# Kernel optimization log

Hardware: AMD Instinct MI355X
Metric: run time of the kernel (lower is better)

The kernel has to match this reference:

```python
import jax, jax.numpy as jnp
import numpy as np


def setup_inputs() -> dict:
    key = jax.random.key(0)
    ks = jax.random.split(key, 6)
    B, C, H, W, Q = 16, 64, 64, 64, 8192
    HID = 256
    K = C * 9  # 576, unfolded channel count and srnet out_dim (co_mat=1)
    feat = jax.random.normal(ks[0], (B, C, H, W), jnp.float32)
    coord = jax.random.uniform(ks[1], (B, Q, 2), jnp.float32) * 2.0 - 1.0  # normalized [-1,1]
    cell = jnp.ones((B, Q, 2), jnp.float32) * (2.0 / 128.0)  # HR cell size for 128-px grid
    w1 = jax.random.normal(ks[2], (3, HID), jnp.float32) / np.sqrt(3.0)
    b1 = jnp.zeros((HID,), jnp.float32)
    w2 = jax.random.normal(ks[3], (HID, HID), jnp.float32) / np.sqrt(float(HID))
    b2 = jnp.zeros((HID,), jnp.float32)
    w3 = jax.random.normal(ks[4], (HID, K), jnp.float32) / np.sqrt(float(HID))
    b3 = jnp.zeros((K,), jnp.float32)
    return {"feat": feat, "coord": coord, "cell": cell,
            "w1": w1, "b1": b1, "w2": w2, "b2": b2, "w3": w3, "b3": b3}


def reference(feat, coord, cell, w1, b1, w2, b2, w3, b3):
    B, C, H, W = feat.shape
    Q = coord.shape[1]
    K = C * 9
    co_mat = 1
    # F.unfold(feat, 3, padding=1).view(B, C*9, H, W): channel-major, kernel pos minor
    padded = jnp.pad(feat, ((0, 0), (0, 0), (1, 1), (1, 1)))
    patches = jnp.stack([padded[:, :, i:i + H, j:j + W]
                         for i in range(3) for j in range(3)], axis=2)  # [B,C,9,H,W]
    featu = patches.reshape(B, K, H * W)
    # shift query coords by half a cell
    coord_ = coord - cell / 2.0
    coord_q = jnp.clip(coord_ + 1e-6, -1.0 + 1e-6, 1.0 - 1e-6)
    # nearest grid_sample, align_corners=False: idx = round(((c+1)*S - 1)/2)
    # coord[...,0] indexes H (grid y after flip), coord[...,1] indexes W (grid x)
    iy = jnp.clip(jnp.round(((coord_q[..., 0] + 1.0) * H - 1.0) / 2.0), 0, H - 1).astype(jnp.int32)
    ix = jnp.clip(jnp.round(((coord_q[..., 1] + 1.0) * W - 1.0) / 2.0), 0, W - 1).astype(jnp.int32)
    lin = iy * W + ix  # [B,Q]
    q_feat = jnp.take_along_axis(featu, lin[:, None, :], axis=2).transpose(0, 2, 1)  # [B,Q,K]
    # q_coord: make_coord value minus half-pixel shift at the nearest index = 2i/S - 1 (exact)
    qy = 2.0 * iy.astype(jnp.float32) / H - 1.0
    qx = 2.0 * ix.astype(jnp.float32) / W - 1.0
    rel_y = (coord_[..., 0] - qy) * (H / 2.0)
    rel_x = (coord_[..., 1] - qx) * (W / 2.0)
    r_rev = cell[..., 0] * (H / 2.0)
    inp = jnp.stack([rel_y, rel_x, r_rev], axis=-1)  # [B,Q,3]
    # srnet MLP: per-query filter of shape [K, co_mat]
    h = jax.nn.relu(inp @ w1 + b1)
    h = jax.nn.relu(h @ w2 + b2)
    wmat = (h @ w3 + b3).reshape(B, Q, K, co_mat)
    # bmm combine: [1,K] @ [K,co_mat] per query
    pred = jnp.einsum('bqk,bqkc->bqc', q_feat, wmat)  # [B,Q,1]
    return pred
```

## Files before the change

kernel.cpp:

```cpp
#include <hip/hip_runtime.h>
#include <hip/hip_bf16.h>

#define BB 16
#define CC 64
#define HH 64
#define WW 64
#define QQ 8192
#define HID 256
#define KK 576
#define HT 66
#define FROW 264

typedef short short8 __attribute__((ext_vector_type(8)));
typedef short sv4    __attribute__((ext_vector_type(4)));
typedef float f32x4  __attribute__((ext_vector_type(4)));

__device__ __forceinline__ short f2bf(float f) {
    union { float f; unsigned u; } v; v.f = f;
    unsigned r = v.u + 0x7fffu + ((v.u >> 16) & 1u);
    return (short)(r >> 16);
}
__device__ __forceinline__ float bf2f(short s) {
    union { unsigned u; float f; } v; v.u = ((unsigned)(unsigned short)s) << 16;
    return v.f;
}
__device__ __forceinline__ void barrier_lds() {
    asm volatile("s_waitcnt lgkmcnt(0)" ::: "memory");
    __builtin_amdgcn_s_barrier();
    asm volatile("" ::: "memory");
}
__device__ __forceinline__ void glld16(const short* g, short* l) {
    __builtin_amdgcn_global_load_lds(
        (const __attribute__((address_space(1))) void*)g,
        (__attribute__((address_space(3))) void*)l, 16, 0, 0);
}

__global__ __launch_bounds__(256) void prep_transpose_k(const float* __restrict__ feat,
                                                        const float* __restrict__ w2,
                                                        const float* __restrict__ w3,
                                                        const float* __restrict__ b3,
                                                        short* __restrict__ featT,
                                                        short* __restrict__ w3cB,
                                                        short* __restrict__ w2cB) {
    __shared__ float ftile[64][65];
    const int t = threadIdx.x;
    const int gidx = blockIdx.x * 256 + t;

    if (gidx < 156672) {
        int kchunk = gidx / 2176;
        int rem = gidx - kchunk * 2176;
        int n = rem >> 3, j = rem & 7;
        int kglob = kchunk * 8 + j;
        int pos = kglob >> 6, c = kglob & 63;
        float v = 0.f;
        if (n < 256)      v = w3[n * KK + c * 9 + pos];
        else if (n == 256) v = b3[c * 9 + pos];
        w3cB[gidx] = f2bf(v);
    }
    if (gidx < 65536) {
        int kchunk = gidx >> 11;
        int rem = gidx & 2047;
        int n = rem >> 3, j = rem & 7;
        int k = kchunk * 8 + j;
        w2cB[gidx] = f2bf(w2[k * 256 + n]);
    }

    const int x = blockIdx.x & 7;
    const int i = blockIdx.x >> 3;
    const int b  = (i < 66) ? (x + 8) : x;
    const int yy = (i < 66) ? i : (i - 66);
    short* out_row = featT + ((b * HT + yy) * HT) * 64;

    if (yy == 0 || yy == HT - 1) {
        for (int idx = t; idx < HT * 64; idx += 256) out_row[idx] = 0;
        return;
    }
    const int y = yy - 1;
    const float* src = feat + ((b * CC) * HH + y) * WW;
#pragma unroll
    for (int i2 = 0; i2 < 16; ++i2) {
        int idx = i2 * 256 + t;
        int c = idx >> 6, xx = idx & 63;
        ftile[c][xx] = src[c * (HH * WW) + xx];
    }
    if (t < 64) out_row[t] = 0;
    else if (t < 128) out_row[(HT - 1) * 64 + (t - 64)] = 0;
    __syncthreads();
#pragma unroll
    for (int i2 = 0; i2 < 16; ++i2) {
        int idx = i2 * 256 + t;
        int xx = idx >> 6, c = idx & 63;
        out_row[(xx + 1) * 64 + c] = f2bf(ftile[c][xx]);
    }
}

#define SSTR 72
__global__ __launch_bounds__(256, 2) void conv_k(const short* __restrict__ featT,
                                                 const short* __restrict__ w3cB,
                                                 short* __restrict__ F) {
    __shared__ short slab[3 * HT * SSTR];
    const int t = threadIdx.x;
    const int wave = t >> 6, lane = t & 63, quad = lane >> 4, ln16 = lane & 15;
    const int x = blockIdx.x & 7;
    const int i0 = blockIdx.x >> 3;
    const int b = (i0 < 64) ? (x + 8) : x;
    const int y = i0 & 63;

    f32x4 acc[4][5];
#pragma unroll
    for (int a = 0; a < 4; ++a)
#pragma unroll
        for (int i = 0; i < 5; ++i) acc[a][i] = (f32x4){0.f, 0.f, 0.f, 0.f};

    short8 bbuf[3][5];
    const short* bbase = w3cB + (quad * 272 + ln16) * 8;
    auto loadB = [&](int st, int slot) {
#pragma unroll
        for (int i = 0; i < 5; ++i) {
            int sub = (i < 4) ? (wave + 4 * i) : 16;
            bbuf[slot][i] = *(const short8*)(bbase + st * 8704 + sub * 128);
        }
    };

    loadB(0, 0);
    loadB(1, 1);

    const short* slabsrc = featT + b * (HT * HT * 64) + y * (HT * 64);
#pragma unroll
    for (int it = 0; it < 7; ++it) {
        int i = it * 256 + t;
        if (i < 1584) {
            short8 v = *(const short8*)(slabsrc + i * 8);
            int row = i >> 3, cs = (i & 7) * 8;
            *(short8*)(&slab[row * SSTR + cs]) = v;
        }
    }
    barrier_lds();

#pragma unroll
    for (int st = 0; st < 18; ++st) {
        if (st < 16) loadB(st + 2, (st + 2) % 3);
        const int pos = st >> 1, ks = st & 1;
        const int di = pos / 3, dj = pos - di * 3;
        short8 af[4];
#pragma unroll
        for (int ms = 0; ms < 4; ++ms)
            af[ms] = *(const short8*)(&slab[(di * HT + ms * 16 + ln16 + dj) * SSTR + ks * 32 + quad * 8]);
#pragma unroll
        for (int i = 0; i < 5; ++i)
#pragma unroll
            for (int ms = 0; ms < 4; ++ms)
                acc[ms][i] = __builtin_amdgcn_mfma_f32_16x16x32_bf16(af[ms], bbuf[st % 3][i], acc[ms][i], 0, 0, 0);
    }

#pragma unroll
    for (int h = 0; h < 2; ++h) {
        if (h) barrier_lds();
#pragma unroll
        for (int i = 0; i < 5; ++i) {
            int sub = (i < 4) ? (wave + 4 * i) : 16;
            int n = sub * 16 + ln16;
            bool store = (i < 4) || (wave == 0 && n < FROW);
            if (store) {
#pragma unroll
                for (int ms2 = 0; ms2 < 2; ++ms2) {
                    int ms = h * 2 + ms2;
#pragma unroll
                    for (int r = 0; r < 4; ++r) {
                        int xl = ms2 * 16 + quad * 4 + r;
                        slab[xl * FROW + n] = f2bf(acc[ms][i][r]);
                    }
                }
            }
        }
        barrier_lds();
        short8* dst = (short8*)(F + ((long)(b * 64 + y) * 64 + h * 32) * FROW);
        const short8* src8 = (const short8*)slab;
#pragma unroll
        for (int it = 0; it < 5; ++it) {
            int idx = it * 256 + t;
            if (idx < (32 * FROW) / 8) dst[idx] = src8[idx];
        }
    }
}

__global__ __launch_bounds__(256, 2) void mlp_k(const float* __restrict__ coord,
                                                const float* __restrict__ cell,
                                                const float* __restrict__ w1,
                                                const float* __restrict__ b1,
                                                const float* __restrict__ b2v,
                                                const short* __restrict__ w2cB,
                                                const short* __restrict__ F,
                                                float* __restrict__ out) {
    __shared__ short HhF[16384];
    __shared__ short FLds[16384];

    const int t = threadIdx.x;
    const int wave = t >> 6, lane = t & 63, quad = lane >> 4, ln16 = lane & 15;
    const int xcd = blockIdx.x & 7;
    const int i0 = blockIdx.x >> 3;
    const int b  = (i0 < 128) ? xcd : (xcd + 8);
    const int qi = i0 & 127;
    const int qbase = b * QQ + qi * 64;

    const int g = qbase + lane;
    const float2 cc = *(const float2*)(coord + g * 2);
    const float2 ce = *(const float2*)(cell + g * 2);

    short8 wbuf[8][4];
    const short* w2base = w2cB + (quad * 256 + wave * 64 + ln16) * 8;
#pragma unroll
    for (int s = 0; s < 8; ++s)
#pragma unroll
        for (int i = 0; i < 4; ++i)
            wbuf[s][i] = *(const short8*)(w2base + s * 8192 + i * 128);
    __builtin_amdgcn_sched_barrier(0);

    const float coy = cc.x - ce.x * 0.5f, cox = cc.y - ce.y * 0.5f;
    const float cqy = fminf(fmaxf(coy + 1e-6f, -0.999999f), 0.999999f);
    const float cqx = fminf(fmaxf(cox + 1e-6f, -0.999999f), 0.999999f);
    int iy = (int)rintf(((cqy + 1.0f) * 64.0f - 1.0f) * 0.5f); iy = min(max(iy, 0), 63);
    int ix = (int)rintf(((cqx + 1.0f) * 64.0f - 1.0f) * 0.5f); ix = min(max(ix, 0), 63);
    const int lin = iy * 64 + ix;
    const float in0 = (coy - ((float)iy * (1.0f / 32.0f) - 1.0f)) * 32.0f;
    const float in1 = (cox - ((float)ix * (1.0f / 32.0f) - 1.0f)) * 32.0f;
    const float in2 = ce.x * 32.0f;

    short8 hv[8];
    const int k0w = wave * 64;
#pragma unroll
    for (int c8 = 0; c8 < 8; ++c8) {
        const int k0 = k0w + c8 * 8;
        f32x4 wa0 = *(const f32x4*)(w1 + k0),       wa1 = *(const f32x4*)(w1 + k0 + 4);
        f32x4 wb0 = *(const f32x4*)(w1 + 256 + k0), wb1 = *(const f32x4*)(w1 + 256 + k0 + 4);
        f32x4 wc0 = *(const f32x4*)(w1 + 512 + k0), wc1 = *(const f32x4*)(w1 + 512 + k0 + 4);
        f32x4 bb0 = *(const f32x4*)(b1 + k0),       bb1 = *(const f32x4*)(b1 + k0 + 4);
#pragma unroll
        for (int jj = 0; jj < 4; ++jj) {
            float v0 = fmaf(in0, wa0[jj], fmaf(in1, wb0[jj], fmaf(in2, wc0[jj], bb0[jj])));
            float v1 = fmaf(in0, wa1[jj], fmaf(in1, wb1[jj], fmaf(in2, wc1[jj], bb1[jj])));
            hv[c8][jj]     = f2bf(fmaxf(v0, 0.f));
            hv[c8][jj + 4] = f2bf(fmaxf(v1, 0.f));
        }
    }
#pragma unroll
    for (int c8 = 0; c8 < 8; ++c8)
        *(short8*)(&HhF[((2 * wave + (c8 >> 2)) * 4 + (c8 & 3)) * 512 + lane * 8]) = hv[c8];
    __builtin_amdgcn_sched_barrier(0);

    const short* Fb = F + (long)b * 4096 * FROW;
    const short fbs = Fb[(long)lin * FROW + 256];
#pragma unroll
    for (int j = 0; j < 8; ++j) {
        const int r = 2 * (wave * 8 + j) + (lane >> 5);
        const int linr = __shfl(lin, r, 64);
        const int colb = ((lane & 31) * 16) ^ ((r & 7) << 4);
        glld16(Fb + (long)linr * FROW + (colb >> 1), &FLds[(wave * 8 + j) * 512]);
    }
    __builtin_amdgcn_sched_barrier(0);

    barrier_lds();

    f32x4 acc2[4][4];
#pragma unroll
    for (int i = 0; i < 4; ++i)
#pragma unroll
        for (int ms = 0; ms < 4; ++ms) acc2[i][ms] = (f32x4){0.f, 0.f, 0.f, 0.f};

#pragma unroll
    for (int s = 0; s < 8; ++s) {
        short8 hf[4];
#pragma unroll
        for (int ms = 0; ms < 4; ++ms)
            hf[ms] = *(const short8*)(&HhF[(s * 4 + quad) * 512 + (ms * 16 + ln16) * 8]);
#pragma unroll
        for (int i = 0; i < 4; ++i)
#pragma unroll
            for (int ms = 0; ms < 4; ++ms)
                acc2[i][ms] = __builtin_amdgcn_mfma_f32_16x16x32_bf16(wbuf[s][i], hf[ms], acc2[i][ms], 0, 0, 0);
    }

    __syncthreads();

    f32x4 b2q[4];
#pragma unroll
    for (int i = 0; i < 4; ++i)
        b2q[i] = *(const f32x4*)(b2v + wave * 64 + i * 16 + quad * 4);

    const float fbv = bf2f(fbs);
    float part[4] = {0.f, 0.f, 0.f, 0.f};
    const char* FLb = (const char*)FLds;
#pragma unroll
    for (int ms = 0; ms < 4; ++ms) {
        const int r = ms * 16 + ln16;
        const int xr = (r & 7) << 4;
        const int rb = r * 512;
#pragma unroll
        for (int i = 0; i < 4; ++i) {
            sv4 fvv = *(const sv4*)(FLb + rb + ((wave * 128 + i * 32 + quad * 8) ^ xr));
#pragma unroll
            for (int r4 = 0; r4 < 4; ++r4)
                part[ms] = fmaf(fmaxf(acc2[i][ms][r4] + b2q[i][r4], 0.f), bf2f(fvv[r4]), part[ms]);
        }
    }
#pragma unroll
    for (int ms = 0; ms < 4; ++ms) {
        part[ms] += __shfl_xor(part[ms], 16, 64);
        part[ms] += __shfl_xor(part[ms], 32, 64);
    }
    barrier_lds();
    float* red = (float*)FLds;
    if (quad == 0) {
#pragma unroll
        for (int ms = 0; ms < 4; ++ms) red[(ms * 16 + ln16) * 4 + wave] = part[ms];
    }
    barrier_lds();
    if (t < 64)
        out[qbase + t] = red[t * 4 + 0] + red[t * 4 + 1] + red[t * 4 + 2] + red[t * 4 + 3] + fbv;
}

extern "C" void kernel_launch(void* const* d_in, const int* in_sizes, int n_in,
                              void* d_out, int out_size, void* d_ws, size_t ws_size,
                              hipStream_t stream) {
    const float* feat  = (const float*)d_in[0];
    const float* coord = (const float*)d_in[1];
    const float* cell  = (const float*)d_in[2];
    const float* w1    = (const float*)d_in[3];
    const float* b1    = (const float*)d_in[4];
    const float* w2    = (const float*)d_in[5];
    const float* b2    = (const float*)d_in[6];
    const float* w3    = (const float*)d_in[7];
    const float* b3    = (const float*)d_in[8];
    float* out = (float*)d_out;

    char* ws = (char*)d_ws;
    short* w3cB  = (short*)(ws);
    short* w2cB  = (short*)(ws + 313344);
    short* featT = (short*)(ws + 444416);
    short* F     = (short*)(ws + 9365504);
    (void)ws_size; (void)in_sizes; (void)n_in; (void)out_size;

    prep_transpose_k<<<BB * HT, 256, 0, stream>>>(feat, w2, w3, b3, featT, w3cB, w2cB);
    conv_k<<<BB * HH, 256, 0, stream>>>(featT, w3cB, F);
    mlp_k<<<(BB * QQ) / 64, 256, 0, stream>>>(coord, cell, w1, b1, b2, w2cB, F, out);
}
```

Before: 143.8 us.

## Process two query blocks per MLP workgroup to reuse loaded w2 fragments

Each mlp_k workgroup now handles 128 queries as two 64-query blocks. The w2 register fragments and b2 are loaded once and reused across both blocks, and the second block's feature gather is issued while the first block's reduction runs. The bias is folded into the accumulator initialisation, and bf16 packing uses the v_cvt_pk_bf16_f32 instruction. The grid is halved, which leaves fewer workgroups to hide latency and adds extra barriers.

```diff
diff --git a/kernel.cpp b/kernel.cpp
--- a/kernel.cpp
+++ b/kernel.cpp
@@ -14,6 +14,7 @@
 typedef short short8 __attribute__((ext_vector_type(8)));
 typedef short sv4    __attribute__((ext_vector_type(4)));
 typedef float f32x4  __attribute__((ext_vector_type(4)));
+typedef int   iv4    __attribute__((ext_vector_type(4)));
 
 __device__ __forceinline__ short f2bf(float f) {
     union { float f; unsigned u; } v; v.f = f;
@@ -23,6 +24,11 @@
 __device__ __forceinline__ float bf2f(short s) {
     union { unsigned u; float f; } v; v.u = ((unsigned)(unsigned short)s) << 16;
     return v.f;
+}
+__device__ __forceinline__ unsigned cvtpk_bf16(float a, float b) {
+    unsigned r;
+    asm("v_cvt_pk_bf16_f32 %0, %1, %2" : "=v"(r) : "v"(a), "v"(b));
+    return r;
 }
 __device__ __forceinline__ void barrier_lds() {
     asm volatile("s_waitcnt lgkmcnt(0)" ::: "memory");
@@ -199,13 +205,14 @@
     const int wave = t >> 6, lane = t & 63, quad = lane >> 4, ln16 = lane & 15;
     const int xcd = blockIdx.x & 7;
     const int i0 = blockIdx.x >> 3;
-    const int b  = (i0 < 128) ? xcd : (xcd + 8);
-    const int qi = i0 & 127;
-    const int qbase = b * QQ + qi * 64;
-
-    const int g = qbase + lane;
-    const float2 cc = *(const float2*)(coord + g * 2);
-    const float2 ce = *(const float2*)(cell + g * 2);
+    const int b  = (i0 < 64) ? xcd : (xcd + 8);
+    const int qp = i0 & 63;
+    const int qbase0 = b * QQ + qp * 128;
+
+    const float2 cc0 = *(const float2*)(coord + (qbase0 + lane) * 2);
+    const float2 ce0 = *(const float2*)(cell + (qbase0 + lane) * 2);
+    const float2 cc1 = *(const float2*)(coord + (qbase0 + 64 + lane) * 2);
+    const float2 ce1 = *(const float2*)(cell + (qbase0 + 64 + lane) * 2);
 
     short8 wbuf[8][4];
     const short* w2base = w2cB + (quad * 256 + wave * 64 + ln16) * 8;
@@ -214,109 +221,138 @@
 #pragma unroll
         for (int i = 0; i < 4; ++i)
             wbuf[s][i] = *(const short8*)(w2base + s * 8192 + i * 128);
-    __builtin_amdgcn_sched_barrier(0);
-
-    const float coy = cc.x - ce.x * 0.5f, cox = cc.y - ce.y * 0.5f;
-    const float cqy = fminf(fmaxf(coy + 1e-6f, -0.999999f), 0.999999f);
-    const float cqx = fminf(fmaxf(cox + 1e-6f, -0.999999f), 0.999999f);
-    int iy = (int)rintf(((cqy + 1.0f) * 64.0f - 1.0f) * 0.5f); iy = min(max(iy, 0), 63);
-    int ix = (int)rintf(((cqx + 1.0f) * 64.0f - 1.0f) * 0.5f); ix = min(max(ix, 0), 63);
-    const int lin = iy * 64 + ix;
-    const float in0 = (coy - ((float)iy * (1.0f / 32.0f) - 1.0f)) * 32.0f;
-    const float in1 = (cox - ((float)ix * (1.0f / 32.0f) - 1.0f)) * 32.0f;
-    const float in2 = ce.x * 32.0f;
-
-    short8 hv[8];
-    const int k0w = wave * 64;
-#pragma unroll
-    for (int c8 = 0; c8 < 8; ++c8) {
-        const int k0 = k0w + c8 * 8;
-        f32x4 wa0 = *(const f32x4*)(w1 + k0),       wa1 = *(const f32x4*)(w1 + k0 + 4);
-        f32x4 wb0 = *(const f32x4*)(w1 + 256 + k0), wb1 = *(const f32x4*)(w1 + 256 + k0 + 4);
-        f32x4 wc0 = *(const f32x4*)(w1 + 512 + k0), wc1 = *(const f32x4*)(w1 + 512 + k0 + 4);
-        f32x4 bb0 = *(const f32x4*)(b1 + k0),       bb1 = *(const f32x4*)(b1 + k0 + 4);
-#pragma unroll
-        for (int jj = 0; jj < 4; ++jj) {
-            float v0 = fmaf(in0, wa0[jj], fmaf(in1, wb0[jj], fmaf(in2, wc0[jj], bb0[jj])));
-            float v1 = fmaf(in0, wa1[jj], fmaf(in1, wb1[jj], fmaf(in2, wc1[jj], bb1[jj])));
-            hv[c8][jj]     = f2bf(fmaxf(v0, 0.f));
-            hv[c8][jj + 4] = f2bf(fmaxf(v1, 0.f));
-        }
-    }
-#pragma unroll
-    for (int c8 = 0; c8 < 8; ++c8)
-        *(short8*)(&HhF[((2 * wave + (c8 >> 2)) * 4 + (c8 & 3)) * 512 + lane * 8]) = hv[c8];
-    __builtin_amdgcn_sched_barrier(0);
-
-    const short* Fb = F + (long)b * 4096 * FROW;
-    const short fbs = Fb[(long)lin * FROW + 256];
-#pragma unroll
-    for (int j = 0; j < 8; ++j) {
-        const int r = 2 * (wave * 8 + j) + (lane >> 5);
-        const int linr = __shfl(lin, r, 64);
-        const int colb = ((lane & 31) * 16) ^ ((r & 7) << 4);
-        glld16(Fb + (long)linr * FROW + (colb >> 1), &FLds[(wave * 8 + j) * 512]);
-    }
-    __builtin_amdgcn_sched_barrier(0);
-
-    barrier_lds();
-
-    f32x4 acc2[4][4];
-#pragma unroll
-    for (int i = 0; i < 4; ++i)
-#pragma unroll
-        for (int ms = 0; ms < 4; ++ms) acc2[i][ms] = (f32x4){0.f, 0.f, 0.f, 0.f};
-
-#pragma unroll
-    for (int s = 0; s < 8; ++s) {
-        short8 hf[4];
-#pragma unroll
-        for (int ms = 0; ms < 4; ++ms)
-            hf[ms] = *(const short8*)(&HhF[(s * 4 + quad) * 512 + (ms * 16 + ln16) * 8]);
-#pragma unroll
-        for (int i = 0; i < 4; ++i)
-#pragma unroll
-            for (int ms = 0; ms < 4; ++ms)
-                acc2[i][ms] = __builtin_amdgcn_mfma_f32_16x16x32_bf16(wbuf[s][i], hf[ms], acc2[i][ms], 0, 0, 0);
-    }
-
-    __syncthreads();
 
     f32x4 b2q[4];
 #pragma unroll
     for (int i = 0; i < 4; ++i)
         b2q[i] = *(const f32x4*)(b2v + wave * 64 + i * 16 + quad * 4);
-
-    const float fbv = bf2f(fbs);
-    float part[4] = {0.f, 0.f, 0.f, 0.f};
-    const char* FLb = (const char*)FLds;
-#pragma unroll
-    for (int ms = 0; ms < 4; ++ms) {
-        const int r = ms * 16 + ln16;
-        const int xr = (r & 7) << 4;
-        const int rb = r * 512;
-#pragma unroll
-        for (int i = 0; i < 4; ++i) {
-            sv4 fvv = *(const sv4*)(FLb + rb + ((wave * 128 + i * 32 + quad * 8) ^ xr));
-#pragma unroll
-            for (int r4 = 0; r4 < 4; ++r4)
-                part[ms] = fmaf(fmaxf(acc2[i][ms][r4] + b2q[i][r4], 0.f), bf2f(fvv[r4]), part[ms]);
-        }
-    }
-#pragma unroll
-    for (int ms = 0; ms < 4; ++ms) {
-        part[ms] += __shfl_xor(part[ms], 16, 64);
-        part[ms] += __shfl_xor(part[ms], 32, 64);
-    }
+    __builtin_amdgcn_sched_barrier(0);
+
+    int lin[2]; float in0[2], in1[2], in2[2];
+#pragma unroll
+    for (int blk = 0; blk < 2; ++blk) {
+        const float2 cc = blk ? cc1 : cc0;
+        const float2 ce = blk ? ce1 : ce0;
+        const float coy = cc.x - ce.x * 0.5f, cox = cc.y - ce.y * 0.5f;
+        const float cqy = fminf(fmaxf(coy + 1e-6f, -0.999999f), 0.999999f);
+        const float cqx = fminf(fmaxf(cox + 1e-6f, -0.999999f), 0.999999f);
+        int iy = (int)rintf(((cqy + 1.0f) * 64.0f - 1.0f) * 0.5f); iy = min(max(iy, 0), 63);
+        int ix = (int)rintf(((cqx + 1.0f) * 64.0f - 1.0f) * 0.5f); ix = min(max(ix, 0), 63);
+        lin[blk] = iy * 64 + ix;
+        in0[blk] = (coy - ((float)iy * (1.0f / 32.0f) - 1.0f)) * 32.0f;
+        in1[blk] = (cox - ((float)ix * (1.0f / 32.0f) - 1.0f)) * 32.0f;
+        in2[blk] = ce.x * 32.0f;
+    }
+    const short* Fb = F + (long)b * 4096 * FROW;
+    const int k0w = wave * 64;
+
+    auto doH1 = [&](int blk) {
+        const float a0 = in0[blk], a1 = in1[blk], a2 = in2[blk];
+#pragma unroll
+        for (int c8 = 0; c8 < 8; ++c8) {
+            const int k0 = k0w + c8 * 8;
+            f32x4 wa0 = *(const f32x4*)(w1 + k0),       wa1 = *(const f32x4*)(w1 + k0 + 4);
+            f32x4 wb0 = *(const f32x4*)(w1 + 256 + k0), wb1 = *(const f32x4*)(w1 + 256 + k0 + 4);
+            f32x4 wc0 = *(const f32x4*)(w1 + 512 + k0), wc1 = *(const f32x4*)(w1 + 512 + k0 + 4);
+            f32x4 bb0 = *(const f32x4*)(b1 + k0),       bb1 = *(const f32x4*)(b1 + k0 + 4);
+            f32x4 v0, v1;
+#pragma unroll
+            for (int jj = 0; jj < 4; ++jj) {
+                v0[jj] = fmaxf(fmaf(a0, wa0[jj], fmaf(a1, wb0[jj], fmaf(a2, wc0[jj], bb0[jj]))), 0.f);
+                v1[jj] = fmaxf(fmaf(a0, wa1[jj], fmaf(a1, wb1[jj], fmaf(a2, wc1[jj], bb1[jj]))), 0.f);
+            }
+            iv4 pk;
+            pk[0] = (int)cvtpk_bf16(v0[0], v0[1]);
+            pk[1] = (int)cvtpk_bf16(v0[2], v0[3]);
+            pk[2] = (int)cvtpk_bf16(v1[0], v1[1]);
+            pk[3] = (int)cvtpk_bf16(v1[2], v1[3]);
+            *(iv4*)(&HhF[((2 * wave + (c8 >> 2)) * 4 + (c8 & 3)) * 512 + lane * 8]) = pk;
+        }
+    };
+    auto doGather = [&](int blk, short& fbs) {
+        fbs = Fb[(long)lin[blk] * FROW + 256];
+#pragma unroll
+        for (int j = 0; j < 8; ++j) {
+            const int r = 2 * (wave * 8 + j) + (lane >> 5);
+            const int linr = __shfl(lin[blk], r, 64);
+            const int colb = ((lane & 31) * 16) ^ ((r & 7) << 4);
+            glld16(Fb + (long)linr * FROW + (colb >> 1), &FLds[(wave * 8 + j) * 512]);
+        }
+    };
+
+    short fbs0, fbs1;
+    doH1(0);
+    __builtin_amdgcn_sched_barrier(0);
+    doGather(0, fbs0);
+    __builtin_amdgcn_sched_barrier(0);
     barrier_lds();
-    float* red = (float*)FLds;
-    if (quad == 0) {
-#pragma unroll
-        for (int ms = 0; ms < 4; ++ms) red[(ms * 16 + ln16) * 4 + wave] = part[ms];
-    }
-    barrier_lds();
-    if (t < 64)
-        out[qbase + t] = red[t * 4 + 0] + red[t * 4 + 1] + red[t * 4 + 2] + red[t * 4 + 3] + fbv;
+
+    f32x4 acc2[4][4];
+#pragma unroll
+    for (int blk = 0; blk < 2; ++blk) {
+#pragma unroll
+        for (int i = 0; i < 4; ++i)
+#pragma unroll
+            for (int ms = 0; ms < 4; ++ms) acc2[i][ms] = b2q[i];
+#pragma unroll
+        for (int s = 0; s < 8; ++s) {
+            short8 hf[4];
+#pragma unroll
+            for (int ms = 0; ms < 4; ++ms)
+                hf[ms] = *(const short8*)(&HhF[(s * 4 + quad) * 512 + (ms * 16 + ln16) * 8]);
+#pragma unroll
+            for (int i = 0; i < 4; ++i)
+#pragma unroll
+                for (int ms = 0; ms < 4; ++ms)
+                    acc2[i][ms] = __builtin_amdgcn_mfma_f32_16x16x32_bf16(wbuf[s][i], hf[ms], acc2[i][ms], 0, 0, 0);
+        }
+
+        __syncthreads();
+
+        const float fbv = bf2f(blk ? fbs1 : fbs0);
+        float part[4] = {0.f, 0.f, 0.f, 0.f};
+        const char* FLb = (const char*)FLds;
+#pragma unroll
+        for (int ms = 0; ms < 4; ++ms) {
+            const int r = ms * 16 + ln16;
+            const int xr = (r & 7) << 4;
+            const int rb = r * 512;
+#pragma unroll
+            for (int i = 0; i < 4; ++i) {
+                sv4 fvv = *(const sv4*)(FLb + rb + ((wave * 128 + i * 32 + quad * 8) ^ xr));
+#pragma unroll
+                for (int r4 = 0; r4 < 4; ++r4)
+                    part[ms] = fmaf(fmaxf(acc2[i][ms][r4], 0.f), bf2f(fvv[r4]), part[ms]);
+            }
+        }
+#pragma unroll
+        for (int ms = 0; ms < 4; ++ms) {
+            part[ms] += __shfl_xor(part[ms], 16, 64);
+            part[ms] += __shfl_xor(part[ms], 32, 64);
+        }
+        barrier_lds();
+
+        if (blk == 0) {
+            doGather(1, fbs1);
+            __builtin_amdgcn_sched_barrier(0);
+        }
+
+        float* red = (float*)HhF;
+        if (quad == 0) {
+#pragma unroll
+            for (int ms = 0; ms < 4; ++ms) red[(ms * 16 + ln16) * 4 + wave] = part[ms];
+        }
+        barrier_lds();
+        if (t < 64)
+            out[qbase0 + blk * 64 + t] = red[t * 4 + 0] + red[t * 4 + 1] + red[t * 4 + 2] + red[t * 4 + 3] + fbv;
+
+        if (blk == 0) {
+            barrier_lds();
+            doH1(1);
+            __builtin_amdgcn_sched_barrier(0);
+            barrier_lds();
+        }
+    }
 }
 
 extern "C" void kernel_launch(void* const* d_in, const int* in_sizes, int n_in,
@@ -342,5 +378,5 @@
 
     prep_transpose_k<<<BB * HT, 256, 0, stream>>>(feat, w2, w3, b3, featT, w3cB, w2cB);
     conv_k<<<BB * HH, 256, 0, stream>>>(featT, w3cB, F);
-    mlp_k<<<(BB * QQ) / 64, 256, 0, stream>>>(coord, cell, w1, b1, b2, w2cB, F, out);
-}
+    mlp_k<<<(BB * QQ) / 128, 256, 0, stream>>>(coord, cell, w1, b1, b2, w2cB, F, out);
+}
```

New measurement: 186.0 us. 29.3% more time.

## Per-wave F gather layout, drop barriers, fold bias into MFMA accumulators

Applied to the files above, without the earlier changes.

The gather of F rows into LDS is reorganised so each wave loads only the 64-column slice it consumes, which lets the post-MFMA __syncthreads and one reduction barrier be replaced by a per-wave vmcnt wait and a separate reduction buffer. The b2 bias now seeds the MFMA accumulators instead of being added in the epilogue. Layer-1 activations are packed to bf16 with the hardware v_cvt_pk_bf16_f32 instruction and stored per chunk, so the hv register array is no longer held. This cuts barrier stalls and ALU work, at the cost of a new swizzle layout that has to match on both the write and read sides, and it swaps the manual round-to-nearest-even conversion for the hardware one.

```diff
diff --git a/kernel.cpp b/kernel.cpp
--- a/kernel.cpp
+++ b/kernel.cpp
@@ -14,6 +14,7 @@
 typedef short short8 __attribute__((ext_vector_type(8)));
 typedef short sv4    __attribute__((ext_vector_type(4)));
 typedef float f32x4  __attribute__((ext_vector_type(4)));
+typedef int   iv4    __attribute__((ext_vector_type(4)));
 
 __device__ __forceinline__ short f2bf(float f) {
     union { float f; unsigned u; } v; v.f = f;
@@ -23,6 +24,11 @@
 __device__ __forceinline__ float bf2f(short s) {
     union { unsigned u; float f; } v; v.u = ((unsigned)(unsigned short)s) << 16;
     return v.f;
+}
+__device__ __forceinline__ unsigned cvtpk_bf16(float a, float b) {
+    unsigned r;
+    asm("v_cvt_pk_bf16_f32 %0, %1, %2" : "=v"(r) : "v"(a), "v"(b));
+    return r;
 }
 __device__ __forceinline__ void barrier_lds() {
     asm volatile("s_waitcnt lgkmcnt(0)" ::: "memory");
@@ -194,6 +200,7 @@
                                                 float* __restrict__ out) {
     __shared__ short HhF[16384];
     __shared__ short FLds[16384];
+    __shared__ float red_s[64][4];
 
     const int t = threadIdx.x;
     const int wave = t >> 6, lane = t & 63, quad = lane >> 4, ln16 = lane & 15;
@@ -214,6 +221,11 @@
 #pragma unroll
         for (int i = 0; i < 4; ++i)
             wbuf[s][i] = *(const short8*)(w2base + s * 8192 + i * 128);
+
+    f32x4 b2q[4];
+#pragma unroll
+    for (int i = 0; i < 4; ++i)
+        b2q[i] = *(const f32x4*)(b2v + wave * 64 + i * 16 + quad * 4);
     __builtin_amdgcn_sched_barrier(0);
 
     const float coy = cc.x - ce.x * 0.5f, cox = cc.y - ce.y * 0.5f;
@@ -226,7 +238,6 @@
     const float in1 = (cox - ((float)ix * (1.0f / 32.0f) - 1.0f)) * 32.0f;
     const float in2 = ce.x * 32.0f;
 
-    short8 hv[8];
     const int k0w = wave * 64;
 #pragma unroll
     for (int c8 = 0; c8 < 8; ++c8) {
@@ -235,28 +246,30 @@
         f32x4 wb0 = *(const f32x4*)(w1 + 256 + k0), wb1 = *(const f32x4*)(w1 + 256 + k0 + 4);
         f32x4 wc0 = *(const f32x4*)(w1 + 512 + k0), wc1 = *(const f32x4*)(w1 + 512 + k0 + 4);
         f32x4 bb0 = *(const f32x4*)(b1 + k0),       bb1 = *(const f32x4*)(b1 + k0 + 4);
+        f32x4 v0, v1;
 #pragma unroll
         for (int jj = 0; jj < 4; ++jj) {
-            float v0 = fmaf(in0, wa0[jj], fmaf(in1, wb0[jj], fmaf(in2, wc0[jj], bb0[jj])));
-            float v1 = fmaf(in0, wa1[jj], fmaf(in1, wb1[jj], fmaf(in2, wc1[jj], bb1[jj])));
-            hv[c8][jj]     = f2bf(fmaxf(v0, 0.f));
-            hv[c8][jj + 4] = f2bf(fmaxf(v1, 0.f));
-        }
-    }
-#pragma unroll
-    for (int c8 = 0; c8 < 8; ++c8)
-        *(short8*)(&HhF[((2 * wave + (c8 >> 2)) * 4 + (c8 & 3)) * 512 + lane * 8]) = hv[c8];
+            v0[jj] = fmaxf(fmaf(in0, wa0[jj], fmaf(in1, wb0[jj], fmaf(in2, wc0[jj], bb0[jj]))), 0.f);
+            v1[jj] = fmaxf(fmaf(in0, wa1[jj], fmaf(in1, wb1[jj], fmaf(in2, wc1[jj], bb1[jj]))), 0.f);
+        }
+        iv4 pk;
+        pk[0] = (int)cvtpk_bf16(v0[0], v0[1]);
+        pk[1] = (int)cvtpk_bf16(v0[2], v0[3]);
+        pk[2] = (int)cvtpk_bf16(v1[0], v1[1]);
+        pk[3] = (int)cvtpk_bf16(v1[2], v1[3]);
+        *(iv4*)(&HhF[((2 * wave + (c8 >> 2)) * 4 + (c8 & 3)) * 512 + lane * 8]) = pk;
+    }
     __builtin_amdgcn_sched_barrier(0);
 
     const short* Fb = F + (long)b * 4096 * FROW;
     const short fbs = Fb[(long)lin * FROW + 256];
-#pragma unroll
-    for (int j = 0; j < 8; ++j) {
-        const int r = 2 * (wave * 8 + j) + (lane >> 5);
-        const int linr = __shfl(lin, r, 64);
-        const int colb = ((lane & 31) * 16) ^ ((r & 7) << 4);
-        glld16(Fb + (long)linr * FROW + (colb >> 1), &FLds[(wave * 8 + j) * 512]);
-    }
+    int linr[8];
+#pragma unroll
+    for (int j = 0; j < 8; ++j) linr[j] = __shfl(lin, 8 * j + (lane >> 3), 64);
+    const int srcoff = wave * 64 + (((lane & 7) ^ (lane >> 3)) << 3);
+#pragma unroll
+    for (int j = 0; j < 8; ++j)
+        glld16(Fb + (long)linr[j] * FROW + srcoff, &FLds[wave * 4096 + j * 512]);
     __builtin_amdgcn_sched_barrier(0);
 
     barrier_lds();
@@ -265,7 +278,7 @@
 #pragma unroll
     for (int i = 0; i < 4; ++i)
 #pragma unroll
-        for (int ms = 0; ms < 4; ++ms) acc2[i][ms] = (f32x4){0.f, 0.f, 0.f, 0.f};
+        for (int ms = 0; ms < 4; ++ms) acc2[i][ms] = b2q[i];
 
 #pragma unroll
     for (int s = 0; s < 8; ++s) {
@@ -280,27 +293,24 @@
                 acc2[i][ms] = __builtin_amdgcn_mfma_f32_16x16x32_bf16(wbuf[s][i], hf[ms], acc2[i][ms], 0, 0, 0);
     }
 
-    __syncthreads();
-
-    f32x4 b2q[4];
-#pragma unroll
-    for (int i = 0; i < 4; ++i)
-        b2q[i] = *(const f32x4*)(b2v + wave * 64 + i * 16 + quad * 4);
+    asm volatile("s_waitcnt vmcnt(0)" ::: "memory");
+    __builtin_amdgcn_sched_barrier(0);
 
     const float fbv = bf2f(fbs);
     float part[4] = {0.f, 0.f, 0.f, 0.f};
-    const char* FLb = (const char*)FLds;
+    const char* FLb = (const char*)FLds + wave * 8192;
 #pragma unroll
     for (int ms = 0; ms < 4; ++ms) {
         const int r = ms * 16 + ln16;
-        const int xr = (r & 7) << 4;
-        const int rb = r * 512;
+        const int rx = r & 7;
+        const int rb = (r >> 3) * 1024 + rx * 128 + (quad & 1) * 8;
 #pragma unroll
         for (int i = 0; i < 4; ++i) {
-            sv4 fvv = *(const sv4*)(FLb + rb + ((wave * 128 + i * 32 + quad * 8) ^ xr));
+            const int ch = (2 * i + (quad >> 1)) ^ rx;
+            sv4 fvv = *(const sv4*)(FLb + rb + ch * 16);
 #pragma unroll
             for (int r4 = 0; r4 < 4; ++r4)
-                part[ms] = fmaf(fmaxf(acc2[i][ms][r4] + b2q[i][r4], 0.f), bf2f(fvv[r4]), part[ms]);
+                part[ms] = fmaf(fmaxf(acc2[i][ms][r4], 0.f), bf2f(fvv[r4]), part[ms]);
         }
     }
 #pragma unroll
@@ -308,15 +318,13 @@
         part[ms] += __shfl_xor(part[ms], 16, 64);
         part[ms] += __shfl_xor(part[ms], 32, 64);
     }
-    barrier_lds();
-    float* red = (float*)FLds;
     if (quad == 0) {
 #pragma unroll
-        for (int ms = 0; ms < 4; ++ms) red[(ms * 16 + ln16) * 4 + wave] = part[ms];
+        for (int ms = 0; ms < 4; ++ms) red_s[ms * 16 + ln16][wave] = part[ms];
     }
     barrier_lds();
     if (t < 64)
-        out[qbase + t] = red[t * 4 + 0] + red[t * 4 + 1] + red[t * 4 + 2] + red[t * 4 + 3] + fbv;
+        out[qbase + t] = red_s[t][0] + red_s[t][1] + red_s[t][2] + red_s[t][3] + fbv;
 }
 
 extern "C" void kernel_launch(void* const* d_in, const int* in_sizes, int n_in,
```

After: 145.6 us. No clear change (+1.2%).
